# Performance work log

Hardware: AMD Instinct MI355X
Metric: run time of the kernel (lower is better)

## Reference

```python
import jax, jax.numpy as jnp
import numpy as np
import math

N = 65536
IN_FEATURES = 64
OUT_FEATURES = 64
N_MODES = 32
N_BASIS = 1 + 2 * N_MODES


def setup_inputs() -> dict:
    key = jax.random.key(0)
    k1, k2 = jax.random.split(key)
    x = jax.random.normal(k1, (N, IN_FEATURES), dtype=jnp.float32)
    coeffs = jax.random.normal(k2, (OUT_FEATURES, IN_FEATURES, N_BASIS), dtype=jnp.float32) * 0.1
    bias = jnp.zeros((OUT_FEATURES,), dtype=jnp.float32)
    return {"x": x, "coeffs": coeffs, "bias": bias}


def reference(x, coeffs, bias):
    # freqs: [modes] = (1..modes) * pi
    freqs = jnp.arange(1, N_MODES + 1, dtype=x.dtype) * jnp.asarray(math.pi, dtype=x.dtype)
    x_flat = x.reshape(-1, IN_FEATURES)                      # [n, i]
    angles = x_flat[..., None] * freqs                       # [n, i, m]
    ones = jnp.ones(x_flat.shape + (1,), dtype=x.dtype)      # [n, i, 1]
    basis = jnp.concatenate([ones, jnp.sin(angles), jnp.cos(angles)], axis=-1)  # [n, i, b]
    out = jnp.einsum('oib,nib->no', coeffs, basis) + bias    # [n, o]
    return out.reshape(*x.shape[:-1], OUT_FEATURES)
```

## Files before the change

kernel.cpp:

```cpp
#include <hip/hip_runtime.h>
#include <hip/hip_bf16.h>


typedef __bf16 bf16x8 __attribute__((ext_vector_type(8)));
typedef float  f32x4  __attribute__((ext_vector_type(4)));

#define NROWS 65536
#define PI_F 3.14159265358979323846f

__global__ __launch_bounds__(256) void fkan_repack(
    const float* __restrict__ coeffs, const float* __restrict__ bias,
    __bf16* __restrict__ Bp, float* __restrict__ bias2) {
  int gid = blockIdx.x * 256 + threadIdx.x;
  int t    = gid & 7;
  int lane = (gid >> 3) & 63;
  int frag = gid >> 9;
  int c = frag & 3;
  int j = (frag >> 2) & 3;
  int m = frag >> 4;
  int q  = lane >> 4;
  int nl = lane & 15;
  int i = j * 16 + q * 4 + (t >> 1);
  int o = c * 16 + nl;
  int b = (t & 1) ? (33 + m) : (1 + m);
  Bp[gid] = (__bf16)coeffs[(o * 64 + i) * 65 + b];

  if (gid < 64) {
    float s = bias[gid];
    for (int ii = 0; ii < 64; ++ii) s += coeffs[(gid * 64 + ii) * 65 + 0];
    bias2[gid] = s;
  }
}

__global__ __launch_bounds__(256) void fkan_main(
    const float* __restrict__ x, const __bf16* __restrict__ Bp,
    const float* __restrict__ bias2, float* __restrict__ out) {
  __shared__ __bf16 Bs[2][8192];

  int tid  = threadIdx.x;
  int wave = tid >> 6;
  int lane = tid & 63;
  int q    = lane >> 4;
  int rl   = lane & 15;
  int row  = blockIdx.x * 64 + wave * 16 + rl;

  float s1[16], c1[16], sm[16], cm[16];
  const float* xrow = x + (size_t)row * 64;
  #pragma unroll
  for (int j = 0; j < 4; ++j) {
    f32x4 v = *(const f32x4*)(xrow + j * 16 + q * 4);
    #pragma unroll
    for (int e = 0; e < 4; ++e) {
      float ss, cc;
      __sincosf(PI_F * v[e], &ss, &cc);
      s1[j * 4 + e] = ss;  c1[j * 4 + e] = cc;
      sm[j * 4 + e] = ss;  cm[j * 4 + e] = cc;
    }
  }

  f32x4 acc[4];
  #pragma unroll
  for (int c = 0; c < 4; ++c) acc[c] = (f32x4){0.f, 0.f, 0.f, 0.f};

  {
    const f32x4* src = (const f32x4*)Bp;
    f32x4* dst = (f32x4*)(&Bs[0][0]);
    #pragma unroll
    for (int k = 0; k < 4; ++k) dst[k * 256 + tid] = src[k * 256 + tid];
  }
  __syncthreads();

  for (int m = 0; m < 32; ++m) {
    int nb = m & 1;
    if (m < 31) {
      const f32x4* src = (const f32x4*)(Bp + (size_t)(m + 1) * 8192);
      f32x4* dst = (f32x4*)(&Bs[nb ^ 1][0]);
      #pragma unroll
      for (int k = 0; k < 4; ++k) dst[k * 256 + tid] = src[k * 256 + tid];
    }

    #pragma unroll
    for (int j = 0; j < 4; ++j) {
      bf16x8 af;
      #pragma unroll
      for (int e = 0; e < 4; ++e) {
        af[2 * e]     = (__bf16)sm[j * 4 + e];
        af[2 * e + 1] = (__bf16)cm[j * 4 + e];
      }
      #pragma unroll
      for (int c = 0; c < 4; ++c) {
        const bf16x8* bf =
            (const bf16x8*)(&Bs[nb][(j * 4 + c) * 512 + lane * 8]);
        acc[c] = __builtin_amdgcn_mfma_f32_16x16x32_bf16(af, *bf, acc[c],
                                                         0, 0, 0);
      }
    }

    #pragma unroll
    for (int p = 0; p < 16; ++p) {
      float ns = fmaf(sm[p], c1[p],  cm[p] * s1[p]);
      float nc = fmaf(cm[p], c1[p], -sm[p] * s1[p]);
      sm[p] = ns;  cm[p] = nc;
    }
    __syncthreads();
  }

  float b2[4];
  #pragma unroll
  for (int c = 0; c < 4; ++c) b2[c] = bias2[c * 16 + rl];
  int orow = blockIdx.x * 64 + wave * 16 + q * 4;
  #pragma unroll
  for (int c = 0; c < 4; ++c) {
    #pragma unroll
    for (int r = 0; r < 4; ++r) {
      out[(size_t)(orow + r) * 64 + c * 16 + rl] = acc[c][r] + b2[c];
    }
  }
}

extern "C" void kernel_launch(void* const* d_in, const int* in_sizes, int n_in,
                              void* d_out, int out_size, void* d_ws, size_t ws_size,
                              hipStream_t stream) {
  const float* x      = (const float*)d_in[0];
  const float* coeffs = (const float*)d_in[1];
  const float* bias   = (const float*)d_in[2];
  float* out = (float*)d_out;

  __bf16* Bp   = (__bf16*)d_ws;
  float* bias2 = (float*)((char*)d_ws + 512 * 1024);

  int n_rows = in_sizes[0] / 64;

  fkan_repack<<<1024, 256, 0, stream>>>(coeffs, bias, Bp, bias2);
  fkan_main<<<n_rows / 64, 256, 0, stream>>>(x, Bp, bias2, out);
}
```

Measured before the change: 137.5 us.

## Switch to 32x32 MFMA tiles with Chebyshev recurrence and async LDS staging

The main kernel now uses 32x32x16 bf16 MFMA with 128 rows per block instead of 16x16x32 with 64 rows, which halves the number of blocks and raises the output tile per wave. The angle-addition rotation becomes a two-term Chebyshev recurrence (2cos·x_k − x_{k-1}) using one FMA per value, with the loop unrolled by two harmonics. Coefficient slices are staged with global_load_lds direct-to-LDS loads, and the repack kernel writes vectorized 8-element fragments. The cost is higher register pressure from five 32-float arrays, which conflicts with the occupancy hint of two blocks per SM. The Chebyshev recurrence may also accumulate more rounding error than the rotation form.

```diff
diff --git a/kernel.cpp b/kernel.cpp
--- a/kernel.cpp
+++ b/kernel.cpp
@@ -4,35 +4,54 @@
 
 typedef __bf16 bf16x8 __attribute__((ext_vector_type(8)));
 typedef float  f32x4  __attribute__((ext_vector_type(4)));
+typedef float  f32x16 __attribute__((ext_vector_type(16)));
 
-#define NROWS 65536
 #define PI_F 3.14159265358979323846f
 
 __global__ __launch_bounds__(256) void fkan_repack(
     const float* __restrict__ coeffs, const float* __restrict__ bias,
     __bf16* __restrict__ Bp, float* __restrict__ bias2) {
-  int gid = blockIdx.x * 256 + threadIdx.x;
-  int t    = gid & 7;
-  int lane = (gid >> 3) & 63;
-  int frag = gid >> 9;
-  int c = frag & 3;
-  int j = (frag >> 2) & 3;
-  int m = frag >> 4;
-  int q  = lane >> 4;
-  int nl = lane & 15;
-  int i = j * 16 + q * 4 + (t >> 1);
-  int o = c * 16 + nl;
-  int b = (t & 1) ? (33 + m) : (1 + m);
-  Bp[gid] = (__bf16)coeffs[(o * 64 + i) * 65 + b];
+  int gid  = blockIdx.x * 256 + threadIdx.x;
+  int lane = gid & 63;
+  int frag = gid >> 6;
+  int m  = frag >> 4;
+  int kc = (frag >> 1) & 7;
+  int cc = frag & 1;
+  int o  = cc * 32 + (lane & 31);
+  int kq = lane >> 5;
 
-  if (gid < 64) {
-    float s = bias[gid];
-    for (int ii = 0; ii < 64; ++ii) s += coeffs[(gid * 64 + ii) * 65 + 0];
-    bias2[gid] = s;
+  bf16x8 v;
+  #pragma unroll
+  for (int t = 0; t < 8; ++t) {
+    int i = kc * 8 + kq * 4 + (t >> 1);
+    int b = (t & 1) ? (33 + m) : (1 + m);
+    v[t] = (__bf16)coeffs[(o * 64 + i) * 65 + b];
+  }
+  *(bf16x8*)(Bp + (size_t)frag * 512 + lane * 8) = v;
+
+  if (blockIdx.x == 0 && threadIdx.x < 64) {
+    int oo = threadIdx.x;
+    float s = bias[oo];
+    #pragma unroll 4
+    for (int ii = 0; ii < 64; ++ii) s += coeffs[(oo * 64 + ii) * 65 + 0];
+    bias2[oo] = s;
   }
 }
 
-__global__ __launch_bounds__(256) void fkan_main(
+__device__ __forceinline__ void stage_slice(const __bf16* __restrict__ Bp,
+                                            __bf16* dst, int m, int wave,
+                                            int lane) {
+  const char* g = (const char*)Bp + (size_t)m * 16384 + wave * 4096 + lane * 16;
+  char* l = (char*)dst + wave * 4096;
+  #pragma unroll
+  for (int r = 0; r < 4; ++r) {
+    __builtin_amdgcn_global_load_lds(
+        (const __attribute__((address_space(1))) void*)(g + r * 1024),
+        (__attribute__((address_space(3))) void*)(l + r * 1024), 16, 0, 0);
+  }
+}
+
+__global__ __launch_bounds__(256, 2) void fkan_main(
     const float* __restrict__ x, const __bf16* __restrict__ Bp,
     const float* __restrict__ bias2, float* __restrict__ out) {
   __shared__ __bf16 Bs[2][8192];
@@ -40,80 +59,91 @@
   int tid  = threadIdx.x;
   int wave = tid >> 6;
   int lane = tid & 63;
-  int q    = lane >> 4;
-  int rl   = lane & 15;
-  int row  = blockIdx.x * 64 + wave * 16 + rl;
+  int kq   = lane >> 5;
+  int cl   = lane & 31;
+  int row  = blockIdx.x * 128 + wave * 32 + cl;
 
-  float s1[16], c1[16], sm[16], cm[16];
-  const float* xrow = x + (size_t)row * 64;
+  float T[32], sp[32], cp[32], sc[32], cc_[32];
+  const float* xrow = x + (size_t)row * 64 + kq * 4;
   #pragma unroll
-  for (int j = 0; j < 4; ++j) {
-    f32x4 v = *(const f32x4*)(xrow + j * 16 + q * 4);
+  for (int kc = 0; kc < 8; ++kc) {
+    f32x4 v = *(const f32x4*)(xrow + kc * 8);
     #pragma unroll
     for (int e = 0; e < 4; ++e) {
-      float ss, cc;
-      __sincosf(PI_F * v[e], &ss, &cc);
-      s1[j * 4 + e] = ss;  c1[j * 4 + e] = cc;
-      sm[j * 4 + e] = ss;  cm[j * 4 + e] = cc;
+      int p = kc * 4 + e;
+      float ss, cs;
+      __sincosf(PI_F * v[e], &ss, &cs);
+      T[p] = 2.0f * cs;
+      sc[p] = ss;  cc_[p] = cs;
+      sp[p] = 0.f; cp[p] = 1.f;
     }
   }
 
-  f32x4 acc[4];
+  f32x16 acc[2];
   #pragma unroll
-  for (int c = 0; c < 4; ++c) acc[c] = (f32x4){0.f, 0.f, 0.f, 0.f};
+  for (int c2 = 0; c2 < 2; ++c2)
+    #pragma unroll
+    for (int r = 0; r < 16; ++r) acc[c2][r] = 0.f;
 
-  {
-    const f32x4* src = (const f32x4*)Bp;
-    f32x4* dst = (f32x4*)(&Bs[0][0]);
-    #pragma unroll
-    for (int k = 0; k < 4; ++k) dst[k * 256 + tid] = src[k * 256 + tid];
-  }
+  stage_slice(Bp, &Bs[0][0], 0, wave, lane);
   __syncthreads();
 
-  for (int m = 0; m < 32; ++m) {
-    int nb = m & 1;
-    if (m < 31) {
-      const f32x4* src = (const f32x4*)(Bp + (size_t)(m + 1) * 8192);
-      f32x4* dst = (f32x4*)(&Bs[nb ^ 1][0]);
-      #pragma unroll
-      for (int k = 0; k < 4; ++k) dst[k * 256 + tid] = src[k * 256 + tid];
-    }
-
+  for (int m = 0; m < 32; m += 2) {
+    if (m + 1 < 32) stage_slice(Bp, &Bs[1][0], m + 1, wave, lane);
     #pragma unroll
-    for (int j = 0; j < 4; ++j) {
+    for (int kc = 0; kc < 8; ++kc) {
       bf16x8 af;
       #pragma unroll
       for (int e = 0; e < 4; ++e) {
-        af[2 * e]     = (__bf16)sm[j * 4 + e];
-        af[2 * e + 1] = (__bf16)cm[j * 4 + e];
+        af[2 * e]     = (__bf16)sc[kc * 4 + e];
+        af[2 * e + 1] = (__bf16)cc_[kc * 4 + e];
       }
       #pragma unroll
-      for (int c = 0; c < 4; ++c) {
-        const bf16x8* bf =
-            (const bf16x8*)(&Bs[nb][(j * 4 + c) * 512 + lane * 8]);
-        acc[c] = __builtin_amdgcn_mfma_f32_16x16x32_bf16(af, *bf, acc[c],
-                                                         0, 0, 0);
+      for (int c2 = 0; c2 < 2; ++c2) {
+        bf16x8 bf = *(const bf16x8*)(&Bs[0][(kc * 2 + c2) * 512 + lane * 8]);
+        acc[c2] = __builtin_amdgcn_mfma_f32_32x32x16_bf16(af, bf, acc[c2],
+                                                          0, 0, 0);
       }
     }
+    #pragma unroll
+    for (int p = 0; p < 32; ++p) {
+      sp[p] = fmaf(T[p], sc[p], -sp[p]);
+      cp[p] = fmaf(T[p], cc_[p], -cp[p]);
+    }
+    __syncthreads();
 
+    if (m + 2 < 32) stage_slice(Bp, &Bs[0][0], m + 2, wave, lane);
     #pragma unroll
-    for (int p = 0; p < 16; ++p) {
-      float ns = fmaf(sm[p], c1[p],  cm[p] * s1[p]);
-      float nc = fmaf(cm[p], c1[p], -sm[p] * s1[p]);
-      sm[p] = ns;  cm[p] = nc;
+    for (int kc = 0; kc < 8; ++kc) {
+      bf16x8 af;
+      #pragma unroll
+      for (int e = 0; e < 4; ++e) {
+        af[2 * e]     = (__bf16)sp[kc * 4 + e];
+        af[2 * e + 1] = (__bf16)cp[kc * 4 + e];
+      }
+      #pragma unroll
+      for (int c2 = 0; c2 < 2; ++c2) {
+        bf16x8 bf = *(const bf16x8*)(&Bs[1][(kc * 2 + c2) * 512 + lane * 8]);
+        acc[c2] = __builtin_amdgcn_mfma_f32_32x32x16_bf16(af, bf, acc[c2],
+                                                          0, 0, 0);
+      }
+    }
+    #pragma unroll
+    for (int p = 0; p < 32; ++p) {
+      sc[p]  = fmaf(T[p], sp[p], -sc[p]);
+      cc_[p] = fmaf(T[p], cp[p], -cc_[p]);
     }
     __syncthreads();
   }
 
-  float b2[4];
+  float* orow = out + (size_t)(blockIdx.x * 128 + wave * 32) * 64;
   #pragma unroll
-  for (int c = 0; c < 4; ++c) b2[c] = bias2[c * 16 + rl];
-  int orow = blockIdx.x * 64 + wave * 16 + q * 4;
-  #pragma unroll
-  for (int c = 0; c < 4; ++c) {
+  for (int c2 = 0; c2 < 2; ++c2) {
+    float b2 = bias2[c2 * 32 + cl];
     #pragma unroll
-    for (int r = 0; r < 4; ++r) {
-      out[(size_t)(orow + r) * 64 + c * 16 + rl] = acc[c][r] + b2[c];
+    for (int r = 0; r < 16; ++r) {
+      int ro = (r & 3) + 8 * (r >> 2) + 4 * kq;
+      orow[(size_t)ro * 64 + c2 * 32 + cl] = acc[c2][r] + b2;
     }
   }
 }
@@ -131,6 +161,6 @@
 
   int n_rows = in_sizes[0] / 64;
 
-  fkan_repack<<<1024, 256, 0, stream>>>(coeffs, bias, Bp, bias2);
-  fkan_main<<<n_rows / 64, 256, 0, stream>>>(x, Bp, bias2, out);
+  fkan_repack<<<128, 256, 0, stream>>>(coeffs, bias, Bp, bias2);
+  fkan_main<<<n_rows / 128, 256, 0, stream>>>(x, Bp, bias2, out);
 }
```

Measured after the change: 114.0 us. 1.21x faster.
